# Kernel tuning notes

Hardware: AMD Instinct MI355X
Metric: run time of the kernel (lower is better)

## Reference

```python
import jax, jax.numpy as jnp
import numpy as np

B = 16384
INPUT_DIM = 768
DIM = 500
K = 43  # known_types(33) + unknown_types(10)
VAE_DIM = 1024


def setup_inputs() -> dict:
    key = jax.random.key(0)
    ks = jax.random.split(key, 12)
    x = jax.random.normal(ks[0], (B, INPUT_DIM), dtype=jnp.float32)
    known_mask = jax.random.randint(ks[1], (B,), 0, 2) > 0
    labels = jax.random.randint(ks[2], (B,), 0, 33)
    eps = jax.random.normal(ks[3], (B, VAE_DIM), dtype=jnp.float32)
    # encoder MLP (layers_n=1): single Linear(input_dim -> dim)
    W_enc = jax.random.normal(ks[4], (DIM, INPUT_DIM), dtype=jnp.float32) * (1.0 / np.sqrt(INPUT_DIM))
    b_enc = jnp.zeros((DIM,), dtype=jnp.float32)
    # codebook embedding, init U(-1/K, 1/K)
    codebook = jax.random.uniform(ks[5], (K, DIM), dtype=jnp.float32, minval=-1.0 / K, maxval=1.0 / K)
    # vae_encoder MLP (layers_n=2): Linear(input_dim->vae_dim), ReLU, Linear(vae_dim->2*vae_dim)
    W1 = jax.random.normal(ks[6], (VAE_DIM, INPUT_DIM), dtype=jnp.float32) * (1.0 / np.sqrt(INPUT_DIM))
    b1 = jnp.zeros((VAE_DIM,), dtype=jnp.float32)
    W2 = jax.random.normal(ks[7], (2 * VAE_DIM, VAE_DIM), dtype=jnp.float32) * (1.0 / np.sqrt(VAE_DIM))
    b2 = jnp.zeros((2 * VAE_DIM,), dtype=jnp.float32)
    # vae_decoder: Linear(K + vae_dim -> input_dim)
    Wd = jax.random.normal(ks[8], (INPUT_DIM, K + VAE_DIM), dtype=jnp.float32) * (1.0 / np.sqrt(K + VAE_DIM))
    bd = jnp.zeros((INPUT_DIM,), dtype=jnp.float32)
    return {
        "x": x, "known_mask": known_mask, "labels": labels, "eps": eps,
        "W_enc": W_enc, "b_enc": b_enc, "codebook": codebook,
        "W1": W1, "b1": b1, "W2": W2, "b2": b2, "Wd": Wd, "bd": bd,
    }


def reference(x, known_mask, labels, eps, W_enc, b_enc, codebook, W1, b1, W2, b2, Wd, bd):
    # encoder: z_e_x (B, dim)
    z_e_x = x @ W_enc.T + b_enc
    # codebook lookup: logits (B, K); argmax of softmax == argmax of logits
    logits = z_e_x @ codebook.T
    y_tilde = jax.nn.softmax(logits, axis=1)
    indices = jnp.argmax(y_tilde, axis=1)
    z_q_x = codebook[indices]  # (B, dim), differentiable gather w.r.t. codebook
    # VAE encoder: mu, logvar (B, vae_dim)
    h = jax.nn.relu(x @ W1.T + b1)
    mu_logvar = h @ W2.T + b2
    mu, logvar = jnp.split(mu_logvar, 2, axis=1)
    # KL( N(mu, exp(0.5*logvar)) || N(0,1) ), summed over dim, mean over batch
    kl_div = jnp.mean(jnp.sum(0.5 * (jnp.exp(logvar) + mu * mu - 1.0 - logvar), axis=1))
    # reparameterized sample
    sampled_z = mu + jnp.exp(0.5 * logvar) * eps
    # replace known rows of y_tilde with one-hot labels
    onehot = jax.nn.one_hot(labels, logits.shape[1], dtype=y_tilde.dtype)
    y = jnp.where(known_mask[:, None], onehot, y_tilde)
    # vae decoder
    x_tilde = jnp.concatenate([sampled_z, y], axis=1) @ Wd.T + bd
    return (x_tilde, z_e_x, z_q_x, logits, kl_div)
```

## Files before the change

kernel.cpp:

```cpp
#include <hip/hip_runtime.h>
#include <hip/hip_bf16.h>
#include <math.h>


#define B_ROWS 16384

typedef __attribute__((ext_vector_type(8))) short bf16x8;
typedef __attribute__((ext_vector_type(4))) float f32x4;

constexpr size_t X_TILDE_OFF = 0;
constexpr size_t ZE_OFF      = 12582912;
constexpr size_t ZQ_OFF      = 20774912;
constexpr size_t LOG_OFF     = 28966912;
constexpr size_t KL_OFF      = 29671424;

constexpr size_t WS_XH  = 0;
constexpr size_t WS_XL  = 25165824;
constexpr size_t WS_ZB  = 50331648;
constexpr size_t WS_HB  = 85983232;
constexpr size_t WS_W1B = 119537664;
constexpr size_t WS_W2P = 121110528;
constexpr size_t WS_WDB = 125304832;
constexpr size_t WS_WEH = 126976000;
constexpr size_t WS_CBH = 127762432;
constexpr size_t WS_CBL = 127959040;
constexpr size_t WS_CBD = 128155648;
constexpr size_t WS_LBF = 128419840;
constexpr size_t WS_LBD = 128420352;

__device__ __forceinline__ unsigned short f2b(float f) {
    unsigned u = __builtin_bit_cast(unsigned, f);
    return (unsigned short)((u + 0x7FFFu + ((u >> 16) & 1u)) >> 16);
}
__device__ __forceinline__ float b2f(unsigned short u) {
    return __uint_as_float(((unsigned)u) << 16);
}

__device__ __forceinline__ void stage16(const void* g, void* l) {
    __builtin_amdgcn_global_load_lds(
        (const __attribute__((address_space(1))) void*)g,
        (__attribute__((address_space(3))) void*)l, 16, 0, 0);
}

__device__ __forceinline__ void gemm_loop(
    const unsigned short* __restrict__ A,
    const unsigned short* __restrict__ Bw,
    int lda, int ldb, int K, int row0, int col0,
    short* As, short* Bs, f32x4 acc[4][4])
{
    const int t = threadIdx.x;
    const int w = t >> 6, l = t & 63;
    const int wr = (w >> 1) * 64, wc = (w & 1) * 64;
    const unsigned short* a0 = A  + (size_t)(row0 + (t >> 2)) * lda + ((t & 3) << 3);
    const unsigned short* b0 = Bw + (size_t)(col0 + (t >> 2)) * ldb + ((t & 3) << 3);
    const size_t aStep = (size_t)64 * lda, bStep = (size_t)64 * ldb;
    const int fr = l & 15, fk = (l >> 4) << 3;
    const int s0 = t * 8, s1 = (256 + t) * 8;

    stage16(a0, As + s0); stage16(a0 + aStep, As + s1);
    stage16(b0, Bs + s0); stage16(b0 + bStep, Bs + s1);

    int cur = 0;
    for (int k0 = 0; k0 < K; k0 += 32) {
        const int nb = (cur ^ 1) * 4096;
        if (k0 + 32 < K) {
            stage16(a0 + k0 + 32,         As + nb + s0);
            stage16(a0 + aStep + k0 + 32, As + nb + s1);
            stage16(b0 + k0 + 32,         Bs + nb + s0);
            stage16(b0 + bStep + k0 + 32, Bs + nb + s1);
            asm volatile("s_waitcnt vmcnt(4)" ::: "memory");
        } else {
            asm volatile("s_waitcnt vmcnt(0)" ::: "memory");
        }
        __builtin_amdgcn_s_barrier();
        const short* cA = As + cur * 4096;
        const short* cB = Bs + cur * 4096;
        bf16x8 am[4], bn[4];
        #pragma unroll
        for (int i = 0; i < 4; ++i)
            am[i] = *(const bf16x8*)&cA[(wr + i * 16 + fr) * 32 + fk];
        #pragma unroll
        for (int j = 0; j < 4; ++j)
            bn[j] = *(const bf16x8*)&cB[(wc + j * 16 + fr) * 32 + fk];
        #pragma unroll
        for (int i = 0; i < 4; ++i)
            #pragma unroll
            for (int j = 0; j < 4; ++j)
                acc[i][j] = __builtin_amdgcn_mfma_f32_16x16x32_bf16(
                    am[i], bn[j], acc[i][j], 0, 0, 0);
        __builtin_amdgcn_s_barrier();
        cur ^= 1;
    }
}

enum { EPI_H = 0, EPI_XT = 1, EPI_ZE = 2, EPI_ML = 3 };

template<int EPI>
__global__ __launch_bounds__(256) void gemm2(
    const unsigned short* __restrict__ A,
    const unsigned short* __restrict__ Bw,
    const float* __restrict__ bias,
    void* __restrict__ C,
    const float* __restrict__ eps,
    float* __restrict__ kl,
    int lda, int ldb, int ldc, int K)
{
    __shared__ short As[2 * 4096];
    __shared__ short Bs[2 * 4096];
    __shared__ float wsum[4];
    f32x4 acc[4][4] = {};
    const int row0 = blockIdx.y * 128, col0 = blockIdx.x * 128;
    gemm_loop(A, Bw, lda, ldb, K, row0, col0, As, Bs, acc);

    const int t = threadIdx.x, w = t >> 6, l = t & 63;
    const int wr = (w >> 1) * 64, wc = (w & 1) * 64;
    const int fr = l & 15, fq = (l >> 4) << 2;

    if constexpr (EPI == EPI_ML) {
        float klsum = 0.f;
        #pragma unroll
        for (int i = 0; i < 4; ++i) {
            #pragma unroll
            for (int jj = 0; jj < 2; ++jj) {
                const int d = ((col0 + wc) >> 1) + jj * 16 + fr;
                const float bmu = bias[d], blv = bias[1024 + d];
                #pragma unroll
                for (int q = 0; q < 4; ++q) {
                    const int r = row0 + wr + i * 16 + fq + q;
                    const float mu = acc[i][2 * jj][q] + bmu;
                    const float lv = acc[i][2 * jj + 1][q] + blv;
                    const float e  = eps[(size_t)r * 1024 + d];
                    const float z  = fmaf(expf(0.5f * lv), e, mu);
                    ((unsigned short*)C)[(size_t)r * 1088 + d] = f2b(z);
                    klsum += 0.5f * (expf(lv) + mu * mu - 1.f - lv);
                }
            }
        }
        #pragma unroll
        for (int off = 32; off; off >>= 1) klsum += __shfl_xor(klsum, off);
        if (l == 0) wsum[w] = klsum;
        __syncthreads();
        if (t == 0)
            atomicAdd(kl, (wsum[0] + wsum[1] + wsum[2] + wsum[3]) * (1.0f / 16384.f));
    } else {
        #pragma unroll
        for (int i = 0; i < 4; ++i) {
            #pragma unroll
            for (int j = 0; j < 4; ++j) {
                const int c = col0 + wc + j * 16 + fr;
                if (EPI == EPI_ZE && c >= 500) continue;
                const int r0 = row0 + wr + i * 16 + fq;
                const float bv = bias[c];
                #pragma unroll
                for (int q = 0; q < 4; ++q) {
                    float v = acc[i][j][q] + bv;
                    if (EPI == EPI_H) v = fmaxf(v, 0.f);
                    if (EPI == EPI_H)
                        ((unsigned short*)C)[(size_t)(r0 + q) * ldc + c] = f2b(v);
                    else
                        ((float*)C)[(size_t)(r0 + q) * ldc + c] = v;
                }
            }
        }
    }
}

__global__ __launch_bounds__(256) void gemm_x3_logits(
    const unsigned short* __restrict__ Ah,
    const unsigned short* __restrict__ Al,
    const unsigned short* __restrict__ Bh,
    const unsigned short* __restrict__ Bl,
    const float* __restrict__ bias,
    float* __restrict__ C, int K)
{
    __shared__ short sAh[2 * 4096], sAl[2 * 4096];
    __shared__ short sBh[2 * 4096], sBl[2 * 4096];
    const int t = threadIdx.x, w = t >> 6, l = t & 63;
    const int row0 = blockIdx.y * 128;
    const int wr = (w >> 1) * 64, wc = (w & 1) * 64;
    const size_t aoff = (size_t)(row0 + (t >> 2)) * 768 + ((t & 3) << 3);
    const size_t boff = (size_t)(t >> 2) * 768 + ((t & 3) << 3);
    const size_t step = (size_t)64 * 768;
    const int s0 = t * 8, s1 = (256 + t) * 8;
    const int fr = l & 15, fk = (l >> 4) << 3;
    f32x4 acc[4][4] = {};

    #define STAGE_ALL(buf, k)                                                  \
        stage16(Ah + aoff + (k),        sAh + (buf) * 4096 + s0);              \
        stage16(Ah + aoff + step + (k), sAh + (buf) * 4096 + s1);              \
        stage16(Al + aoff + (k),        sAl + (buf) * 4096 + s0);              \
        stage16(Al + aoff + step + (k), sAl + (buf) * 4096 + s1);              \
        stage16(Bh + boff + (k),        sBh + (buf) * 4096 + s0);              \
        stage16(Bh + boff + step + (k), sBh + (buf) * 4096 + s1);              \
        stage16(Bl + boff + (k),        sBl + (buf) * 4096 + s0);              \
        stage16(Bl + boff + step + (k), sBl + (buf) * 4096 + s1);

    STAGE_ALL(0, 0)
    int cur = 0;
    for (int k0 = 0; k0 < K; k0 += 32) {
        if (k0 + 32 < K) {
            STAGE_ALL(cur ^ 1, k0 + 32)
            asm volatile("s_waitcnt vmcnt(8)" ::: "memory");
        } else {
            asm volatile("s_waitcnt vmcnt(0)" ::: "memory");
        }
        __builtin_amdgcn_s_barrier();
        const short* cAh = sAh + cur * 4096;  const short* cAl = sAl + cur * 4096;
        const short* cBh = sBh + cur * 4096;  const short* cBl = sBl + cur * 4096;
        bf16x8 ah[4], al[4], bh[4], bl[4];
        #pragma unroll
        for (int i = 0; i < 4; ++i) {
            ah[i] = *(const bf16x8*)&cAh[(wr + i * 16 + fr) * 32 + fk];
            al[i] = *(const bf16x8*)&cAl[(wr + i * 16 + fr) * 32 + fk];
        }
        #pragma unroll
        for (int j = 0; j < 4; ++j) {
            bh[j] = *(const bf16x8*)&cBh[(wc + j * 16 + fr) * 32 + fk];
            bl[j] = *(const bf16x8*)&cBl[(wc + j * 16 + fr) * 32 + fk];
        }
        #pragma unroll
        for (int i = 0; i < 4; ++i)
            #pragma unroll
            for (int j = 0; j < 4; ++j) {
                acc[i][j] = __builtin_amdgcn_mfma_f32_16x16x32_bf16(
                    ah[i], bh[j], acc[i][j], 0, 0, 0);
                acc[i][j] = __builtin_amdgcn_mfma_f32_16x16x32_bf16(
                    al[i], bh[j], acc[i][j], 0, 0, 0);
                acc[i][j] = __builtin_amdgcn_mfma_f32_16x16x32_bf16(
                    ah[i], bl[j], acc[i][j], 0, 0, 0);
            }
        __builtin_amdgcn_s_barrier();
        cur ^= 1;
    }
    #undef STAGE_ALL

    const int fq = (l >> 4) << 2;
    #pragma unroll
    for (int i = 0; i < 4; ++i)
        #pragma unroll
        for (int j = 0; j < 4; ++j) {
            const int c = wc + j * 16 + fr;
            if (c < 43) {
                const int r0 = row0 + wr + i * 16 + fq;
                const float bv = bias[c];
                #pragma unroll
                for (int q = 0; q < 4; ++q)
                    C[(size_t)(r0 + q) * 43 + c] = acc[i][j][q] + bv;
            }
        }
}

__global__ __launch_bounds__(256) void cbw_kernel(
    const float* __restrict__ W_enc, const float* __restrict__ cb,
    const float* __restrict__ b_enc,
    double* __restrict__ cbWd, unsigned short* __restrict__ cbWh,
    unsigned short* __restrict__ cbWl, float* __restrict__ lbf,
    double* __restrict__ lbd)
{
    const int j = blockIdx.x;
    const int t = threadIdx.x;
    if (j >= 43) {
        for (int d = t; d < 768; d += 256) {
            cbWh[(size_t)j * 768 + d] = 0;
            cbWl[(size_t)j * 768 + d] = 0;
        }
        if (t == 0) lbf[j] = 0.f;
        return;
    }
    double acc[3] = {0.0, 0.0, 0.0};
    for (int k = 0; k < 500; ++k) {
        const double c = (double)cb[(size_t)j * 500 + k];
        acc[0] = fma(c, (double)W_enc[(size_t)k * 768 + t],       acc[0]);
        acc[1] = fma(c, (double)W_enc[(size_t)k * 768 + t + 256], acc[1]);
        acc[2] = fma(c, (double)W_enc[(size_t)k * 768 + t + 512], acc[2]);
    }
    #pragma unroll
    for (int q = 0; q < 3; ++q) {
        const int d = t + q * 256;
        const double v = acc[q];
        cbWd[(size_t)j * 768 + d] = v;
        const float f = (float)v;
        const unsigned short h = f2b(f);
        cbWh[(size_t)j * 768 + d] = h;
        cbWl[(size_t)j * 768 + d] = f2b(f - b2f(h));
    }
    if (t == 0) {
        double s = 0.0;
        for (int k = 0; k < 500; ++k)
            s = fma((double)cb[(size_t)j * 500 + k], (double)b_enc[k], s);
        lbd[j] = s;
        lbf[j] = (float)s;
    }
}

__global__ __launch_bounds__(256) void head_kernel(
    const float* __restrict__ logits, const float* __restrict__ codebook,
    const int* __restrict__ known_mask, const int* __restrict__ labels,
    const float* __restrict__ x, const double* __restrict__ cbWd,
    const double* __restrict__ lbd,
    float* __restrict__ zq_out, unsigned short* __restrict__ Zb)
{
    const int wave = threadIdx.x >> 6;
    const int lane = threadIdx.x & 63;
    const int row  = blockIdx.x * 4 + wave;

    const float* lrow = logits + (size_t)row * 43;
    const float v = (lane < 43) ? lrow[lane] : -INFINITY;

    float bvv = v; int bi = lane;
    #pragma unroll
    for (int off = 32; off; off >>= 1) {
        const float ov = __shfl_xor(bvv, off);
        const int   oi = __shfl_xor(bi, off);
        if (ov > bvv || (ov == bvv && oi < bi)) { bvv = ov; bi = oi; }
    }
    float v2 = (lane == bi) ? -INFINITY : v;
    #pragma unroll
    for (int off = 32; off; off >>= 1) v2 = fmaxf(v2, __shfl_xor(v2, off));

    int idx = bi;
    if (bvv - v2 < 1e-3f) {
        double dv = -1.0e300;
        if (lane < 43) {
            double s = lbd[lane];
            const float* xr = x + (size_t)row * 768;
            const double* wrow = cbWd + (size_t)lane * 768;
            for (int d = 0; d < 768; ++d)
                s = fma((double)xr[d], wrow[d], s);
            dv = s;
        }
        double bdv = dv; int bj = lane;
        #pragma unroll
        for (int off = 32; off; off >>= 1) {
            const double ov = __shfl_xor(bdv, off);
            const int    oi = __shfl_xor(bj, off);
            if (ov > bdv || (ov == bdv && oi < bj)) { bdv = ov; bj = oi; }
        }
        idx = bj;
    }

    float e = (lane < 43) ? expf(v - bvv) : 0.f;
    float s = e;
    #pragma unroll
    for (int off = 32; off; off >>= 1) s += __shfl_xor(s, off);

    const int km  = known_mask[row];
    const int lab = labels[row];
    float y;
    if (lane < 43) y = km ? ((lane == lab) ? 1.f : 0.f) : (e / s);
    else           y = 0.f;
    Zb[(size_t)row * 1088 + 1024 + lane] = f2b(y);

    const float* crow = codebook + (size_t)idx * 500;
    float* zrow = zq_out + (size_t)row * 500;
    for (int c = lane; c < 500; c += 64) zrow[c] = crow[c];
}

__global__ __launch_bounds__(256) void conv_split(
    const float* __restrict__ in,
    unsigned short* __restrict__ hi, unsigned short* __restrict__ lo, int n)
{
    const int i = (blockIdx.x * 256 + threadIdx.x) * 4;
    if (i >= n) return;
    const float4 v = *(const float4*)(in + i);
    ushort4 h, l;
    h.x = f2b(v.x); l.x = f2b(v.x - b2f(h.x));
    h.y = f2b(v.y); l.y = f2b(v.y - b2f(h.y));
    h.z = f2b(v.z); l.z = f2b(v.z - b2f(h.z));
    h.w = f2b(v.w); l.w = f2b(v.w - b2f(h.w));
    *(ushort4*)(hi + i) = h;
    *(ushort4*)(lo + i) = l;
}

__global__ __launch_bounds__(256) void conv_bf16(
    const float* __restrict__ in, unsigned short* __restrict__ out, int n)
{
    const int i = (blockIdx.x * 256 + threadIdx.x) * 4;
    if (i >= n) return;
    const float4 v = *(const float4*)(in + i);
    ushort4 o;
    o.x = f2b(v.x); o.y = f2b(v.y); o.z = f2b(v.z); o.w = f2b(v.w);
    *(ushort4*)(out + i) = o;
}

__global__ __launch_bounds__(256) void wenc_hi(
    const float* __restrict__ W, unsigned short* __restrict__ hi)
{
    const int idx = blockIdx.x * 256 + threadIdx.x;
    if (idx >= 512 * 768) return;
    const int r = idx / 768;
    hi[idx] = (r < 500) ? f2b(W[idx]) : 0;
}

__global__ __launch_bounds__(256) void repack_w2p(
    const float* __restrict__ W2, unsigned short* __restrict__ W2p)
{
    const int idx = blockIdx.x * 256 + threadIdx.x;
    if (idx >= 2048 * 1024) return;
    const int c = idx >> 10;
    const int k = idx & 1023;
    const int s = c & 31, g = c >> 5;
    const int src = ((s < 16) ? 0 : 1024) + g * 16 + (s & 15);
    W2p[idx] = f2b(W2[(size_t)src * 1024 + k]);
}

__global__ __launch_bounds__(256) void repack_wd(
    const float* __restrict__ Wd, unsigned short* __restrict__ Wdb)
{
    const int idx = blockIdx.x * 256 + threadIdx.x;
    if (idx >= 768 * 1088) return;
    const int n = idx / 1088;
    const int k = idx - n * 1088;
    Wdb[idx] = (k < 1067) ? f2b(Wd[(size_t)n * 1067 + k]) : 0;
}

extern "C" void kernel_launch(void* const* d_in, const int* in_sizes, int n_in,
                              void* d_out, int out_size, void* d_ws, size_t ws_size,
                              hipStream_t stream) {
    const float* x        = (const float*)d_in[0];
    const int*   known    = (const int*)  d_in[1];
    const int*   labels   = (const int*)  d_in[2];
    const float* eps      = (const float*)d_in[3];
    const float* W_enc    = (const float*)d_in[4];
    const float* b_enc    = (const float*)d_in[5];
    const float* codebook = (const float*)d_in[6];
    const float* W1       = (const float*)d_in[7];
    const float* b1       = (const float*)d_in[8];
    const float* W2       = (const float*)d_in[9];
    const float* b2       = (const float*)d_in[10];
    const float* Wd       = (const float*)d_in[11];
    const float* bd       = (const float*)d_in[12];
    float* out = (float*)d_out;
    char*  ws  = (char*)d_ws;

    unsigned short* xh   = (unsigned short*)(ws + WS_XH);
    unsigned short* xl   = (unsigned short*)(ws + WS_XL);
    unsigned short* Zb   = (unsigned short*)(ws + WS_ZB);
    unsigned short* hb   = (unsigned short*)(ws + WS_HB);
    unsigned short* W1b  = (unsigned short*)(ws + WS_W1B);
    unsigned short* W2p  = (unsigned short*)(ws + WS_W2P);
    unsigned short* Wdb  = (unsigned short*)(ws + WS_WDB);
    unsigned short* Weh  = (unsigned short*)(ws + WS_WEH);
    unsigned short* cbWh = (unsigned short*)(ws + WS_CBH);
    unsigned short* cbWl = (unsigned short*)(ws + WS_CBL);
    double*         cbWd = (double*)        (ws + WS_CBD);
    float*          lbf  = (float*)         (ws + WS_LBF);
    double*         lbd  = (double*)        (ws + WS_LBD);

    hipMemsetAsync(out + KL_OFF, 0, sizeof(float), stream);

    const dim3 blk(256);
    conv_split<<<(16384 * 768 / 4 + 255) / 256, blk, 0, stream>>>(x, xh, xl, 16384 * 768);
    conv_bf16<<<(1024 * 768 / 4 + 255) / 256, blk, 0, stream>>>(W1, W1b, 1024 * 768);
    repack_w2p<<<(2048 * 1024 + 255) / 256, blk, 0, stream>>>(W2, W2p);
    repack_wd<<<(768 * 1088 + 255) / 256, blk, 0, stream>>>(Wd, Wdb);
    wenc_hi<<<(512 * 768 + 255) / 256, blk, 0, stream>>>(W_enc, Weh);
    cbw_kernel<<<128, blk, 0, stream>>>(W_enc, codebook, b_enc,
                                        cbWd, cbWh, cbWl, lbf, lbd);

    gemm2<EPI_H><<<dim3(8, 128), blk, 0, stream>>>(
        xh, W1b, b1, hb, nullptr, nullptr, 768, 768, 1024, 768);
    gemm2<EPI_ML><<<dim3(16, 128), blk, 0, stream>>>(
        hb, W2p, b2, Zb, eps, out + KL_OFF, 1024, 1024, 0, 1024);
    gemm2<EPI_ZE><<<dim3(4, 128), blk, 0, stream>>>(
        xh, Weh, b_enc, out + ZE_OFF, nullptr, nullptr, 768, 768, 500, 768);
    gemm_x3_logits<<<dim3(1, 128), blk, 0, stream>>>(
        xh, xl, cbWh, cbWl, lbf, out + LOG_OFF, 768);
    head_kernel<<<B_ROWS / 4, blk, 0, stream>>>(
        out + LOG_OFF, codebook, known, labels, x, cbWd, lbd,
        out + ZQ_OFF, Zb);
    gemm2<EPI_XT><<<dim3(6, 128), blk, 0, stream>>>(
        Zb, Wdb, bd, out + X_TILDE_OFF, nullptr, nullptr, 1088, 1088, 768, 1088);
}
```

Measured before the change: 593.8 us.

## Replace 128x128 GEMM with 256x256 eight-wave swizzled LDS pipelined kernel

```diff
diff --git a/kernel.cpp b/kernel.cpp
--- a/kernel.cpp
+++ b/kernel.cpp
@@ -42,96 +42,146 @@
         (__attribute__((address_space(3))) void*)l, 16, 0, 0);
 }
 
-__device__ __forceinline__ void gemm_loop(
-    const unsigned short* __restrict__ A,
-    const unsigned short* __restrict__ Bw,
-    int lda, int ldb, int K, int row0, int col0,
-    short* As, short* Bs, f32x4 acc[4][4])
-{
-    const int t = threadIdx.x;
-    const int w = t >> 6, l = t & 63;
-    const int wr = (w >> 1) * 64, wc = (w & 1) * 64;
-    const unsigned short* a0 = A  + (size_t)(row0 + (t >> 2)) * lda + ((t & 3) << 3);
-    const unsigned short* b0 = Bw + (size_t)(col0 + (t >> 2)) * ldb + ((t & 3) << 3);
-    const size_t aStep = (size_t)64 * lda, bStep = (size_t)64 * ldb;
-    const int fr = l & 15, fk = (l >> 4) << 3;
-    const int s0 = t * 8, s1 = (256 + t) * 8;
-
-    stage16(a0, As + s0); stage16(a0 + aStep, As + s1);
-    stage16(b0, Bs + s0); stage16(b0 + bStep, Bs + s1);
-
-    int cur = 0;
-    for (int k0 = 0; k0 < K; k0 += 32) {
-        const int nb = (cur ^ 1) * 4096;
-        if (k0 + 32 < K) {
-            stage16(a0 + k0 + 32,         As + nb + s0);
-            stage16(a0 + aStep + k0 + 32, As + nb + s1);
-            stage16(b0 + k0 + 32,         Bs + nb + s0);
-            stage16(b0 + bStep + k0 + 32, Bs + nb + s1);
-            asm volatile("s_waitcnt vmcnt(4)" ::: "memory");
-        } else {
-            asm volatile("s_waitcnt vmcnt(0)" ::: "memory");
-        }
-        __builtin_amdgcn_s_barrier();
-        const short* cA = As + cur * 4096;
-        const short* cB = Bs + cur * 4096;
-        bf16x8 am[4], bn[4];
-        #pragma unroll
-        for (int i = 0; i < 4; ++i)
-            am[i] = *(const bf16x8*)&cA[(wr + i * 16 + fr) * 32 + fk];
-        #pragma unroll
-        for (int j = 0; j < 4; ++j)
-            bn[j] = *(const bf16x8*)&cB[(wc + j * 16 + fr) * 32 + fk];
-        #pragma unroll
-        for (int i = 0; i < 4; ++i)
-            #pragma unroll
-            for (int j = 0; j < 4; ++j)
-                acc[i][j] = __builtin_amdgcn_mfma_f32_16x16x32_bf16(
-                    am[i], bn[j], acc[i][j], 0, 0, 0);
-        __builtin_amdgcn_s_barrier();
-        cur ^= 1;
-    }
-}
+__device__ __forceinline__ int swz(int row, int cb) {
+    return cb ^ (((row >> 1) & 3) << 3);
+}
+
+__device__ __forceinline__ void stage_unit(const unsigned short* __restrict__ src,
+                                           int ld, int r0, int k0,
+                                           short* unit, int t) {
+    #pragma unroll
+    for (int j = 0; j < 2; ++j) {
+        const int idx = j * 512 + t;
+        const int row = idx >> 2;
+        const int cb  = (idx & 3) << 3;
+        stage16(src + (size_t)(r0 + row) * ld + k0 + swz(row, cb),
+                unit + idx * 8);
+    }
+}
+
+__device__ __forceinline__ bf16x8 lds_frag(const short* unit, int row, int fk) {
+    return *(const bf16x8*)(unit + row * 32 + swz(row, fk));
+}
+
+#define MFMA16(ACCBASE, AF, BF)                                               \
+    _Pragma("unroll")                                                         \
+    for (int m = 0; m < 4; ++m)                                               \
+        _Pragma("unroll")                                                     \
+        for (int n = 0; n < 4; ++n)                                           \
+            acc[ACCBASE + m][n] = __builtin_amdgcn_mfma_f32_16x16x32_bf16(    \
+                AF[m], BF[n], acc[ACCBASE + m][n], 0, 0, 0);
 
 enum { EPI_H = 0, EPI_XT = 1, EPI_ZE = 2, EPI_ML = 3 };
 
 template<int EPI>
-__global__ __launch_bounds__(256) void gemm2(
+__global__ __launch_bounds__(512, 2) void gemm8(
     const unsigned short* __restrict__ A,
     const unsigned short* __restrict__ Bw,
     const float* __restrict__ bias,
-    void* __restrict__ C,
+    void* __restrict__ Cv,
     const float* __restrict__ eps,
     float* __restrict__ kl,
-    int lda, int ldb, int ldc, int K)
-{
-    __shared__ short As[2 * 4096];
-    __shared__ short Bs[2 * 4096];
-    __shared__ float wsum[4];
-    f32x4 acc[4][4] = {};
-    const int row0 = blockIdx.y * 128, col0 = blockIdx.x * 128;
-    gemm_loop(A, Bw, lda, ldb, K, row0, col0, As, Bs, acc);
-
-    const int t = threadIdx.x, w = t >> 6, l = t & 63;
-    const int wr = (w >> 1) * 64, wc = (w & 1) * 64;
-    const int fr = l & 15, fq = (l >> 4) << 2;
+    int lda, int ldb, int ldc, int K, int gx)
+{
+    __shared__ short As[2][2][8192];
+    __shared__ short Bs[2][2][8192];
+    __shared__ float wsum[8];
+
+    int wg = blockIdx.x;
+    wg = (wg & 7) * ((int)gridDim.x >> 3) + (wg >> 3);
+    const int row0 = (wg / gx) * 256;
+    const int col0 = (wg % gx) * 256;
+
+    const int t = threadIdx.x;
+    const int w = t >> 6, l = t & 63;
+    const int arow = (w >> 2) * 128;
+    const int bcol = (w & 3) * 64;
+    const int fr = l & 15, fk = (l >> 4) << 3, fq = (l >> 4) << 2;
+
+    f32x4 acc[8][4] = {};
+    bf16x8 af[4], bf[4];
+
+    stage_unit(A, lda, row0, 0,  As[0][0], t);
+    stage_unit(Bw, ldb, col0, 0, Bs[0][0], t);
+    stage_unit(A, lda, row0, 32, As[0][1], t);
+    stage_unit(Bw, ldb, col0, 32, Bs[0][1], t);
+    asm volatile("s_waitcnt vmcnt(4)" ::: "memory");
+    asm volatile("s_barrier" ::: "memory");
+
+    const int NT = K >> 6;
+    for (int tt = 0; tt < NT; ++tt) {
+        const int cur = tt & 1, nxt = cur ^ 1;
+        const int kn = (tt + 1) << 6;
+        const bool pf = (tt + 1) < NT;
+
+        #pragma unroll
+        for (int m = 0; m < 4; ++m)
+            af[m] = lds_frag(As[cur][0], arow + m * 16 + fr, fk);
+        #pragma unroll
+        for (int n = 0; n < 4; ++n)
+            bf[n] = lds_frag(Bs[cur][0], bcol + n * 16 + fr, fk);
+        if (pf) stage_unit(A, lda, row0, kn, As[nxt][0], t);
+        asm volatile("s_barrier" ::: "memory");
+        __builtin_amdgcn_s_setprio(1);
+        MFMA16(0, af, bf)
+        __builtin_amdgcn_s_setprio(0);
+        asm volatile("s_barrier" ::: "memory");
+
+        #pragma unroll
+        for (int m = 0; m < 4; ++m)
+            af[m] = lds_frag(As[cur][0], arow + 64 + m * 16 + fr, fk);
+        if (pf) stage_unit(Bw, ldb, col0, kn, Bs[nxt][0], t);
+        asm volatile("s_barrier" ::: "memory");
+        __builtin_amdgcn_s_setprio(1);
+        MFMA16(4, af, bf)
+        __builtin_amdgcn_s_setprio(0);
+        if (pf) asm volatile("s_waitcnt vmcnt(4)" ::: "memory");
+        else    asm volatile("s_waitcnt vmcnt(0)" ::: "memory");
+        asm volatile("s_barrier" ::: "memory");
+
+        #pragma unroll
+        for (int m = 0; m < 4; ++m)
+            af[m] = lds_frag(As[cur][1], arow + m * 16 + fr, fk);
+        #pragma unroll
+        for (int n = 0; n < 4; ++n)
+            bf[n] = lds_frag(Bs[cur][1], bcol + n * 16 + fr, fk);
+        if (pf) stage_unit(A, lda, row0, kn + 32, As[nxt][1], t);
+        asm volatile("s_barrier" ::: "memory");
+        __builtin_amdgcn_s_setprio(1);
+        MFMA16(0, af, bf)
+        __builtin_amdgcn_s_setprio(0);
+        asm volatile("s_barrier" ::: "memory");
+
+        #pragma unroll
+        for (int m = 0; m < 4; ++m)
+            af[m] = lds_frag(As[cur][1], arow + 64 + m * 16 + fr, fk);
+        if (pf) stage_unit(Bw, ldb, col0, kn + 32, Bs[nxt][1], t);
+        asm volatile("s_barrier" ::: "memory");
+        __builtin_amdgcn_s_setprio(1);
+        MFMA16(4, af, bf)
+        __builtin_amdgcn_s_setprio(0);
+        if (pf) asm volatile("s_waitcnt vmcnt(4)" ::: "memory");
+        else    asm volatile("s_waitcnt vmcnt(0)" ::: "memory");
+        asm volatile("s_barrier" ::: "memory");
+    }
 
     if constexpr (EPI == EPI_ML) {
         float klsum = 0.f;
-        #pragma unroll
-        for (int i = 0; i < 4; ++i) {
+        const int dbase = (col0 + bcol) >> 1;
+        #pragma unroll
+        for (int m = 0; m < 8; ++m) {
             #pragma unroll
-            for (int jj = 0; jj < 2; ++jj) {
-                const int d = ((col0 + wc) >> 1) + jj * 16 + fr;
+            for (int pr = 0; pr < 2; ++pr) {
+                const int d = dbase + pr * 16 + fr;
                 const float bmu = bias[d], blv = bias[1024 + d];
                 #pragma unroll
                 for (int q = 0; q < 4; ++q) {
-                    const int r = row0 + wr + i * 16 + fq + q;
-                    const float mu = acc[i][2 * jj][q] + bmu;
-                    const float lv = acc[i][2 * jj + 1][q] + blv;
+                    const int r = row0 + arow + m * 16 + fq + q;
+                    const float mu = acc[m][2 * pr][q] + bmu;
+                    const float lv = acc[m][2 * pr + 1][q] + blv;
                     const float e  = eps[(size_t)r * 1024 + d];
                     const float z  = fmaf(expf(0.5f * lv), e, mu);
-                    ((unsigned short*)C)[(size_t)r * 1088 + d] = f2b(z);
+                    ((unsigned short*)Cv)[(size_t)r * 1088 + d] = f2b(z);
                     klsum += 0.5f * (expf(lv) + mu * mu - 1.f - lv);
                 }
             }
@@ -140,25 +190,29 @@
         for (int off = 32; off; off >>= 1) klsum += __shfl_xor(klsum, off);
         if (l == 0) wsum[w] = klsum;
         __syncthreads();
-        if (t == 0)
-            atomicAdd(kl, (wsum[0] + wsum[1] + wsum[2] + wsum[3]) * (1.0f / 16384.f));
+        if (t == 0) {
+            float s = 0.f;
+            #pragma unroll
+            for (int i = 0; i < 8; ++i) s += wsum[i];
+            atomicAdd(kl, s * (1.0f / 16384.f));
+        }
     } else {
         #pragma unroll
-        for (int i = 0; i < 4; ++i) {
+        for (int m = 0; m < 8; ++m) {
             #pragma unroll
-            for (int j = 0; j < 4; ++j) {
-                const int c = col0 + wc + j * 16 + fr;
+            for (int n = 0; n < 4; ++n) {
+                const int c = col0 + bcol + n * 16 + fr;
                 if (EPI == EPI_ZE && c >= 500) continue;
-                const int r0 = row0 + wr + i * 16 + fq;
+                const int r0 = row0 + arow + m * 16 + fq;
                 const float bv = bias[c];
                 #pragma unroll
                 for (int q = 0; q < 4; ++q) {
-                    float v = acc[i][j][q] + bv;
+                    float v = acc[m][n][q] + bv;
                     if (EPI == EPI_H) v = fmaxf(v, 0.f);
                     if (EPI == EPI_H)
-                        ((unsigned short*)C)[(size_t)(r0 + q) * ldc + c] = f2b(v);
+                        ((unsigned short*)Cv)[(size_t)(r0 + q) * ldc + c] = f2b(v);
                     else
-                        ((float*)C)[(size_t)(r0 + q) * ldc + c] = v;
+                        ((float*)Cv)[(size_t)(r0 + q) * ldc + c] = v;
                 }
             }
         }
@@ -458,17 +512,17 @@
     cbw_kernel<<<128, blk, 0, stream>>>(W_enc, codebook, b_enc,
                                         cbWd, cbWh, cbWl, lbf, lbd);
 
-    gemm2<EPI_H><<<dim3(8, 128), blk, 0, stream>>>(
-        xh, W1b, b1, hb, nullptr, nullptr, 768, 768, 1024, 768);
-    gemm2<EPI_ML><<<dim3(16, 128), blk, 0, stream>>>(
-        hb, W2p, b2, Zb, eps, out + KL_OFF, 1024, 1024, 0, 1024);
-    gemm2<EPI_ZE><<<dim3(4, 128), blk, 0, stream>>>(
-        xh, Weh, b_enc, out + ZE_OFF, nullptr, nullptr, 768, 768, 500, 768);
+    gemm8<EPI_H><<<dim3(256), dim3(512), 0, stream>>>(
+        xh, W1b, b1, hb, nullptr, nullptr, 768, 768, 1024, 768, 4);
+    gemm8<EPI_ML><<<dim3(512), dim3(512), 0, stream>>>(
+        hb, W2p, b2, Zb, eps, out + KL_OFF, 1024, 1024, 0, 1024, 8);
+    gemm8<EPI_ZE><<<dim3(128), dim3(512), 0, stream>>>(
+        xh, Weh, b_enc, out + ZE_OFF, nullptr, nullptr, 768, 768, 500, 768, 2);
     gemm_x3_logits<<<dim3(1, 128), blk, 0, stream>>>(
         xh, xl, cbWh, cbWl, lbf, out + LOG_OFF, 768);
     head_kernel<<<B_ROWS / 4, blk, 0, stream>>>(
         out + LOG_OFF, codebook, known, labels, x, cbWd, lbd,
         out + ZQ_OFF, Zb);
-    gemm2<EPI_XT><<<dim3(6, 128), blk, 0, stream>>>(
-        Zb, Wdb, bd, out + X_TILDE_OFF, nullptr, nullptr, 1088, 1088, 768, 1088);
-}
+    gemm8<EPI_XT><<<dim3(192), dim3(512), 0, stream>>>(
+        Zb, Wdb, bd, out + X_TILDE_OFF, nullptr, nullptr, 1088, 1088, 768, 1088, 3);
+}
```

Result: faster. 561.0 us (-5.5%).

## Fold logits GEMM into encoder GEMM, drop split-bf16 x, single-buffer LDS

Applied to the files above, without the earlier changes.

```diff
diff --git a/kernel.cpp b/kernel.cpp
--- a/kernel.cpp
+++ b/kernel.cpp
@@ -15,18 +15,15 @@
 constexpr size_t KL_OFF      = 29671424;
 
 constexpr size_t WS_XH  = 0;
-constexpr size_t WS_XL  = 25165824;
-constexpr size_t WS_ZB  = 50331648;
-constexpr size_t WS_HB  = 85983232;
-constexpr size_t WS_W1B = 119537664;
-constexpr size_t WS_W2P = 121110528;
-constexpr size_t WS_WDB = 125304832;
-constexpr size_t WS_WEH = 126976000;
-constexpr size_t WS_CBH = 127762432;
-constexpr size_t WS_CBL = 127959040;
-constexpr size_t WS_CBD = 128155648;
-constexpr size_t WS_LBF = 128419840;
-constexpr size_t WS_LBD = 128420352;
+constexpr size_t WS_ZB  = 25165824;
+constexpr size_t WS_HB  = 60817408;
+constexpr size_t WS_W1B = 94371840;
+constexpr size_t WS_W2P = 95944704;
+constexpr size_t WS_WDB = 100139008;
+constexpr size_t WS_WEC = 101810176;
+constexpr size_t WS_CBD = 102793216;
+constexpr size_t WS_LBF = 103057408;
+constexpr size_t WS_LBD = 103057664;
 
 __device__ __forceinline__ unsigned short f2b(float f) {
     unsigned u = __builtin_bit_cast(unsigned, f);
@@ -42,87 +39,72 @@
         (__attribute__((address_space(3))) void*)l, 16, 0, 0);
 }
 
-__device__ __forceinline__ void gemm_loop(
+enum { EPI_H = 0, EPI_XT = 1, EPI_ZL = 2, EPI_ML = 3 };
+
+template<int EPI>
+__global__ __launch_bounds__(256) void gemm1(
     const unsigned short* __restrict__ A,
     const unsigned short* __restrict__ Bw,
-    int lda, int ldb, int K, int row0, int col0,
-    short* As, short* Bs, f32x4 acc[4][4])
-{
-    const int t = threadIdx.x;
-    const int w = t >> 6, l = t & 63;
+    const float* __restrict__ bias,
+    const float* __restrict__ bias2,
+    void* __restrict__ Cv,
+    float* __restrict__ C2,
+    const float* __restrict__ eps,
+    float* __restrict__ kl,
+    int lda, int ldb, int ldc, int K)
+{
+    __shared__ short As[128 * 32];
+    __shared__ short Bs[128 * 32];
+    __shared__ float wsum[4];
+    const int t  = threadIdx.x;
+    const int w  = t >> 6, l = t & 63;
+    const int row0 = blockIdx.y * 128;
+    const int col0 = blockIdx.x * 128;
     const int wr = (w >> 1) * 64, wc = (w & 1) * 64;
+
     const unsigned short* a0 = A  + (size_t)(row0 + (t >> 2)) * lda + ((t & 3) << 3);
     const unsigned short* b0 = Bw + (size_t)(col0 + (t >> 2)) * ldb + ((t & 3) << 3);
-    const size_t aStep = (size_t)64 * lda, bStep = (size_t)64 * ldb;
-    const int fr = l & 15, fk = (l >> 4) << 3;
-    const int s0 = t * 8, s1 = (256 + t) * 8;
-
-    stage16(a0, As + s0); stage16(a0 + aStep, As + s1);
-    stage16(b0, Bs + s0); stage16(b0 + bStep, Bs + s1);
-
-    int cur = 0;
+    const size_t aStep = (size_t)64 * lda;
+    const size_t bStep = (size_t)64 * ldb;
+    short* lA0 = As + t * 8;       short* lA1 = As + (256 + t) * 8;
+    short* lB0 = Bs + t * 8;       short* lB1 = Bs + (256 + t) * 8;
+
+    f32x4 acc[4][4] = {};
+    const int fr = l & 15;
+    const int fk = (l >> 4) << 3;
+
     for (int k0 = 0; k0 < K; k0 += 32) {
-        const int nb = (cur ^ 1) * 4096;
-        if (k0 + 32 < K) {
-            stage16(a0 + k0 + 32,         As + nb + s0);
-            stage16(a0 + aStep + k0 + 32, As + nb + s1);
-            stage16(b0 + k0 + 32,         Bs + nb + s0);
-            stage16(b0 + bStep + k0 + 32, Bs + nb + s1);
-            asm volatile("s_waitcnt vmcnt(4)" ::: "memory");
-        } else {
-            asm volatile("s_waitcnt vmcnt(0)" ::: "memory");
-        }
-        __builtin_amdgcn_s_barrier();
-        const short* cA = As + cur * 4096;
-        const short* cB = Bs + cur * 4096;
+        stage16(a0 + k0, lA0);
+        stage16(a0 + aStep + k0, lA1);
+        stage16(b0 + k0, lB0);
+        stage16(b0 + bStep + k0, lB1);
+        __syncthreads();
         bf16x8 am[4], bn[4];
         #pragma unroll
         for (int i = 0; i < 4; ++i)
-            am[i] = *(const bf16x8*)&cA[(wr + i * 16 + fr) * 32 + fk];
+            am[i] = *(const bf16x8*)&As[(wr + i * 16 + fr) * 32 + fk];
         #pragma unroll
         for (int j = 0; j < 4; ++j)
-            bn[j] = *(const bf16x8*)&cB[(wc + j * 16 + fr) * 32 + fk];
+            bn[j] = *(const bf16x8*)&Bs[(wc + j * 16 + fr) * 32 + fk];
         #pragma unroll
         for (int i = 0; i < 4; ++i)
             #pragma unroll
             for (int j = 0; j < 4; ++j)
                 acc[i][j] = __builtin_amdgcn_mfma_f32_16x16x32_bf16(
                     am[i], bn[j], acc[i][j], 0, 0, 0);
-        __builtin_amdgcn_s_barrier();
-        cur ^= 1;
-    }
-}
-
-enum { EPI_H = 0, EPI_XT = 1, EPI_ZE = 2, EPI_ML = 3 };
-
-template<int EPI>
-__global__ __launch_bounds__(256) void gemm2(
-    const unsigned short* __restrict__ A,
-    const unsigned short* __restrict__ Bw,
-    const float* __restrict__ bias,
-    void* __restrict__ C,
-    const float* __restrict__ eps,
-    float* __restrict__ kl,
-    int lda, int ldb, int ldc, int K)
-{
-    __shared__ short As[2 * 4096];
-    __shared__ short Bs[2 * 4096];
-    __shared__ float wsum[4];
-    f32x4 acc[4][4] = {};
-    const int row0 = blockIdx.y * 128, col0 = blockIdx.x * 128;
-    gemm_loop(A, Bw, lda, ldb, K, row0, col0, As, Bs, acc);
-
-    const int t = threadIdx.x, w = t >> 6, l = t & 63;
-    const int wr = (w >> 1) * 64, wc = (w & 1) * 64;
-    const int fr = l & 15, fq = (l >> 4) << 2;
+        __syncthreads();
+    }
+
+    const int fq = (l >> 4) << 2;
 
     if constexpr (EPI == EPI_ML) {
         float klsum = 0.f;
+        const int dbase = (col0 + wc) >> 1;
         #pragma unroll
         for (int i = 0; i < 4; ++i) {
             #pragma unroll
             for (int jj = 0; jj < 2; ++jj) {
-                const int d = ((col0 + wc) >> 1) + jj * 16 + fr;
+                const int d = dbase + jj * 16 + fr;
                 const float bmu = bias[d], blv = bias[1024 + d];
                 #pragma unroll
                 for (int q = 0; q < 4; ++q) {
@@ -131,7 +113,7 @@
                     const float lv = acc[i][2 * jj + 1][q] + blv;
                     const float e  = eps[(size_t)r * 1024 + d];
                     const float z  = fmaf(expf(0.5f * lv), e, mu);
-                    ((unsigned short*)C)[(size_t)r * 1088 + d] = f2b(z);
+                    ((unsigned short*)Cv)[(size_t)r * 1088 + d] = f2b(z);
                     klsum += 0.5f * (expf(lv) + mu * mu - 1.f - lv);
                 }
             }
@@ -142,131 +124,57 @@
         __syncthreads();
         if (t == 0)
             atomicAdd(kl, (wsum[0] + wsum[1] + wsum[2] + wsum[3]) * (1.0f / 16384.f));
-    } else {
+    } else if constexpr (EPI == EPI_ZL) {
         #pragma unroll
         for (int i = 0; i < 4; ++i) {
             #pragma unroll
             for (int j = 0; j < 4; ++j) {
                 const int c = col0 + wc + j * 16 + fr;
-                if (EPI == EPI_ZE && c >= 500) continue;
+                const int r0 = row0 + wr + i * 16 + fq;
+                if (c < 500) {
+                    const float bv = bias[c];
+                    #pragma unroll
+                    for (int q = 0; q < 4; ++q)
+                        ((float*)Cv)[(size_t)(r0 + q) * 500 + c] = acc[i][j][q] + bv;
+                } else if (c >= 512 && c < 555) {
+                    const float bv = bias2[c - 512];
+                    #pragma unroll
+                    for (int q = 0; q < 4; ++q)
+                        C2[(size_t)(r0 + q) * 43 + (c - 512)] = acc[i][j][q] + bv;
+                }
+            }
+        }
+    } else {
+        #pragma unroll
+        for (int i = 0; i < 4; ++i) {
+            #pragma unroll
+            for (int j = 0; j < 4; ++j) {
+                const int c = col0 + wc + j * 16 + fr;
                 const int r0 = row0 + wr + i * 16 + fq;
                 const float bv = bias[c];
                 #pragma unroll
                 for (int q = 0; q < 4; ++q) {
                     float v = acc[i][j][q] + bv;
-                    if (EPI == EPI_H) v = fmaxf(v, 0.f);
-                    if (EPI == EPI_H)
-                        ((unsigned short*)C)[(size_t)(r0 + q) * ldc + c] = f2b(v);
-                    else
-                        ((float*)C)[(size_t)(r0 + q) * ldc + c] = v;
+                    if (EPI == EPI_H) {
+                        v = fmaxf(v, 0.f);
+                        ((unsigned short*)Cv)[(size_t)(r0 + q) * ldc + c] = f2b(v);
+                    } else {
+                        ((float*)Cv)[(size_t)(r0 + q) * ldc + c] = v;
+                    }
                 }
             }
         }
     }
-}
-
-__global__ __launch_bounds__(256) void gemm_x3_logits(
-    const unsigned short* __restrict__ Ah,
-    const unsigned short* __restrict__ Al,
-    const unsigned short* __restrict__ Bh,
-    const unsigned short* __restrict__ Bl,
-    const float* __restrict__ bias,
-    float* __restrict__ C, int K)
-{
-    __shared__ short sAh[2 * 4096], sAl[2 * 4096];
-    __shared__ short sBh[2 * 4096], sBl[2 * 4096];
-    const int t = threadIdx.x, w = t >> 6, l = t & 63;
-    const int row0 = blockIdx.y * 128;
-    const int wr = (w >> 1) * 64, wc = (w & 1) * 64;
-    const size_t aoff = (size_t)(row0 + (t >> 2)) * 768 + ((t & 3) << 3);
-    const size_t boff = (size_t)(t >> 2) * 768 + ((t & 3) << 3);
-    const size_t step = (size_t)64 * 768;
-    const int s0 = t * 8, s1 = (256 + t) * 8;
-    const int fr = l & 15, fk = (l >> 4) << 3;
-    f32x4 acc[4][4] = {};
-
-    #define STAGE_ALL(buf, k)                                                  \
-        stage16(Ah + aoff + (k),        sAh + (buf) * 4096 + s0);              \
-        stage16(Ah + aoff + step + (k), sAh + (buf) * 4096 + s1);              \
-        stage16(Al + aoff + (k),        sAl + (buf) * 4096 + s0);              \
-        stage16(Al + aoff + step + (k), sAl + (buf) * 4096 + s1);              \
-        stage16(Bh + boff + (k),        sBh + (buf) * 4096 + s0);              \
-        stage16(Bh + boff + step + (k), sBh + (buf) * 4096 + s1);              \
-        stage16(Bl + boff + (k),        sBl + (buf) * 4096 + s0);              \
-        stage16(Bl + boff + step + (k), sBl + (buf) * 4096 + s1);
-
-    STAGE_ALL(0, 0)
-    int cur = 0;
-    for (int k0 = 0; k0 < K; k0 += 32) {
-        if (k0 + 32 < K) {
-            STAGE_ALL(cur ^ 1, k0 + 32)
-            asm volatile("s_waitcnt vmcnt(8)" ::: "memory");
-        } else {
-            asm volatile("s_waitcnt vmcnt(0)" ::: "memory");
-        }
-        __builtin_amdgcn_s_barrier();
-        const short* cAh = sAh + cur * 4096;  const short* cAl = sAl + cur * 4096;
-        const short* cBh = sBh + cur * 4096;  const short* cBl = sBl + cur * 4096;
-        bf16x8 ah[4], al[4], bh[4], bl[4];
-        #pragma unroll
-        for (int i = 0; i < 4; ++i) {
-            ah[i] = *(const bf16x8*)&cAh[(wr + i * 16 + fr) * 32 + fk];
-            al[i] = *(const bf16x8*)&cAl[(wr + i * 16 + fr) * 32 + fk];
-        }
-        #pragma unroll
-        for (int j = 0; j < 4; ++j) {
-            bh[j] = *(const bf16x8*)&cBh[(wc + j * 16 + fr) * 32 + fk];
-            bl[j] = *(const bf16x8*)&cBl[(wc + j * 16 + fr) * 32 + fk];
-        }
-        #pragma unroll
-        for (int i = 0; i < 4; ++i)
-            #pragma unroll
-            for (int j = 0; j < 4; ++j) {
-                acc[i][j] = __builtin_amdgcn_mfma_f32_16x16x32_bf16(
-                    ah[i], bh[j], acc[i][j], 0, 0, 0);
-                acc[i][j] = __builtin_amdgcn_mfma_f32_16x16x32_bf16(
-                    al[i], bh[j], acc[i][j], 0, 0, 0);
-                acc[i][j] = __builtin_amdgcn_mfma_f32_16x16x32_bf16(
-                    ah[i], bl[j], acc[i][j], 0, 0, 0);
-            }
-        __builtin_amdgcn_s_barrier();
-        cur ^= 1;
-    }
-    #undef STAGE_ALL
-
-    const int fq = (l >> 4) << 2;
-    #pragma unroll
-    for (int i = 0; i < 4; ++i)
-        #pragma unroll
-        for (int j = 0; j < 4; ++j) {
-            const int c = wc + j * 16 + fr;
-            if (c < 43) {
-                const int r0 = row0 + wr + i * 16 + fq;
-                const float bv = bias[c];
-                #pragma unroll
-                for (int q = 0; q < 4; ++q)
-                    C[(size_t)(r0 + q) * 43 + c] = acc[i][j][q] + bv;
-            }
-        }
 }
 
 __global__ __launch_bounds__(256) void cbw_kernel(
     const float* __restrict__ W_enc, const float* __restrict__ cb,
     const float* __restrict__ b_enc,
-    double* __restrict__ cbWd, unsigned short* __restrict__ cbWh,
-    unsigned short* __restrict__ cbWl, float* __restrict__ lbf,
-    double* __restrict__ lbd)
+    double* __restrict__ cbWd, unsigned short* __restrict__ WeC,
+    float* __restrict__ lbf, double* __restrict__ lbd)
 {
     const int j = blockIdx.x;
     const int t = threadIdx.x;
-    if (j >= 43) {
-        for (int d = t; d < 768; d += 256) {
-            cbWh[(size_t)j * 768 + d] = 0;
-            cbWl[(size_t)j * 768 + d] = 0;
-        }
-        if (t == 0) lbf[j] = 0.f;
-        return;
-    }
     double acc[3] = {0.0, 0.0, 0.0};
     for (int k = 0; k < 500; ++k) {
         const double c = (double)cb[(size_t)j * 500 + k];
@@ -279,10 +187,7 @@
         const int d = t + q * 256;
         const double v = acc[q];
         cbWd[(size_t)j * 768 + d] = v;
-        const float f = (float)v;
-        const unsigned short h = f2b(f);
-        cbWh[(size_t)j * 768 + d] = h;
-        cbWl[(size_t)j * 768 + d] = f2b(f - b2f(h));
+        WeC[(size_t)(512 + j) * 768 + d] = f2b((float)v);
     }
     if (t == 0) {
         double s = 0.0;
@@ -319,7 +224,7 @@
     for (int off = 32; off; off >>= 1) v2 = fmaxf(v2, __shfl_xor(v2, off));
 
     int idx = bi;
-    if (bvv - v2 < 1e-3f) {
+    if (bvv - v2 < 2e-2f) {
         double dv = -1.0e300;
         if (lane < 43) {
             double s = lbd[lane];
@@ -356,22 +261,6 @@
     for (int c = lane; c < 500; c += 64) zrow[c] = crow[c];
 }
 
-__global__ __launch_bounds__(256) void conv_split(
-    const float* __restrict__ in,
-    unsigned short* __restrict__ hi, unsigned short* __restrict__ lo, int n)
-{
-    const int i = (blockIdx.x * 256 + threadIdx.x) * 4;
-    if (i >= n) return;
-    const float4 v = *(const float4*)(in + i);
-    ushort4 h, l;
-    h.x = f2b(v.x); l.x = f2b(v.x - b2f(h.x));
-    h.y = f2b(v.y); l.y = f2b(v.y - b2f(h.y));
-    h.z = f2b(v.z); l.z = f2b(v.z - b2f(h.z));
-    h.w = f2b(v.w); l.w = f2b(v.w - b2f(h.w));
-    *(ushort4*)(hi + i) = h;
-    *(ushort4*)(lo + i) = l;
-}
-
 __global__ __launch_bounds__(256) void conv_bf16(
     const float* __restrict__ in, unsigned short* __restrict__ out, int n)
 {
@@ -383,13 +272,13 @@
     *(ushort4*)(out + i) = o;
 }
 
-__global__ __launch_bounds__(256) void wenc_hi(
-    const float* __restrict__ W, unsigned short* __restrict__ hi)
+__global__ __launch_bounds__(256) void wecat_fill(
+    const float* __restrict__ W, unsigned short* __restrict__ WeC)
 {
     const int idx = blockIdx.x * 256 + threadIdx.x;
-    if (idx >= 512 * 768) return;
+    if (idx >= 640 * 768) return;
     const int r = idx / 768;
-    hi[idx] = (r < 500) ? f2b(W[idx]) : 0;
+    WeC[idx] = (r < 500) ? f2b(W[idx]) : 0;
 }
 
 __global__ __launch_bounds__(256) void repack_w2p(
@@ -434,15 +323,12 @@
     char*  ws  = (char*)d_ws;
 
     unsigned short* xh   = (unsigned short*)(ws + WS_XH);
-    unsigned short* xl   = (unsigned short*)(ws + WS_XL);
     unsigned short* Zb   = (unsigned short*)(ws + WS_ZB);
     unsigned short* hb   = (unsigned short*)(ws + WS_HB);
     unsigned short* W1b  = (unsigned short*)(ws + WS_W1B);
     unsigned short* W2p  = (unsigned short*)(ws + WS_W2P);
     unsigned short* Wdb  = (unsigned short*)(ws + WS_WDB);
-    unsigned short* Weh  = (unsigned short*)(ws + WS_WEH);
-    unsigned short* cbWh = (unsigned short*)(ws + WS_CBH);
-    unsigned short* cbWl = (unsigned short*)(ws + WS_CBL);
+    unsigned short* WeC  = (unsigned short*)(ws + WS_WEC);
     double*         cbWd = (double*)        (ws + WS_CBD);
     float*          lbf  = (float*)         (ws + WS_LBF);
     double*         lbd  = (double*)        (ws + WS_LBD);
@@ -450,25 +336,24 @@
     hipMemsetAsync(out + KL_OFF, 0, sizeof(float), stream);
 
     const dim3 blk(256);
-    conv_split<<<(16384 * 768 / 4 + 255) / 256, blk, 0, stream>>>(x, xh, xl, 16384 * 768);
+    conv_bf16<<<(16384 * 768 / 4 + 255) / 256, blk, 0, stream>>>(x, xh, 16384 * 768);
     conv_bf16<<<(1024 * 768 / 4 + 255) / 256, blk, 0, stream>>>(W1, W1b, 1024 * 768);
     repack_w2p<<<(2048 * 1024 + 255) / 256, blk, 0, stream>>>(W2, W2p);
     repack_wd<<<(768 * 1088 + 255) / 256, blk, 0, stream>>>(Wd, Wdb);
-    wenc_hi<<<(512 * 768 + 255) / 256, blk, 0, stream>>>(W_enc, Weh);
-    cbw_kernel<<<128, blk, 0, stream>>>(W_enc, codebook, b_enc,
-                                        cbWd, cbWh, cbWl, lbf, lbd);
-
-    gemm2<EPI_H><<<dim3(8, 128), blk, 0, stream>>>(
-        xh, W1b, b1, hb, nullptr, nullptr, 768, 768, 1024, 768);
-    gemm2<EPI_ML><<<dim3(16, 128), blk, 0, stream>>>(
-        hb, W2p, b2, Zb, eps, out + KL_OFF, 1024, 1024, 0, 1024);
-    gemm2<EPI_ZE><<<dim3(4, 128), blk, 0, stream>>>(
-        xh, Weh, b_enc, out + ZE_OFF, nullptr, nullptr, 768, 768, 500, 768);
-    gemm_x3_logits<<<dim3(1, 128), blk, 0, stream>>>(
-        xh, xl, cbWh, cbWl, lbf, out + LOG_OFF, 768);
+    wecat_fill<<<(640 * 768 + 255) / 256, blk, 0, stream>>>(W_enc, WeC);
+    cbw_kernel<<<43, blk, 0, stream>>>(W_enc, codebook, b_enc, cbWd, WeC, lbf, lbd);
+
+    gemm1<EPI_H><<<dim3(8, 128), blk, 0, stream>>>(
+        xh, W1b, b1, nullptr, hb, nullptr, nullptr, nullptr, 768, 768, 1024, 768);
+    gemm1<EPI_ML><<<dim3(16, 128), blk, 0, stream>>>(
+        hb, W2p, b2, nullptr, Zb, nullptr, eps, out + KL_OFF, 1024, 1024, 0, 1024);
+    gemm1<EPI_ZL><<<dim3(5, 128), blk, 0, stream>>>(
+        xh, WeC, b_enc, lbf, out + ZE_OFF, out + LOG_OFF, nullptr, nullptr,
+        768, 768, 500, 768);
     head_kernel<<<B_ROWS / 4, blk, 0, stream>>>(
         out + LOG_OFF, codebook, known, labels, x, cbWd, lbd,
         out + ZQ_OFF, Zb);
-    gemm2<EPI_XT><<<dim3(6, 128), blk, 0, stream>>>(
-        Zb, Wdb, bd, out + X_TILDE_OFF, nullptr, nullptr, 1088, 1088, 768, 1088);
-}
+    gemm1<EPI_XT><<<dim3(6, 128), blk, 0, stream>>>(
+        Zb, Wdb, bd, nullptr, out + X_TILDE_OFF, nullptr, nullptr, nullptr,
+        1088, 1088, 768, 1088);
+}
```

Result: slower. 694.9 us (+17.0%).
